# Kernel tuning notes

Hardware: AMD Instinct MI355X
Metric: run time of the kernel (lower is better)

Reference implementation:

```python
import jax, jax.numpy as jnp
import numpy as np

N_NODES = 50000
N_EDGES = 625000
HIDDEN = 128
NUM_GRAPHS = 128
EPS = 1e-5


def setup_inputs() -> dict:
    key = jax.random.key(0)
    ks = jax.random.split(key, 8)
    node = jax.random.normal(ks[0], (N_NODES, HIDDEN), dtype=jnp.float32)
    edge_index = jax.random.randint(ks[1], (2, N_EDGES), 0, N_NODES, dtype=jnp.int64)
    edge_attr = jax.random.uniform(ks[2], (N_EDGES,), dtype=jnp.float32)
    batch_ptr = jnp.sort(jax.random.randint(ks[3], (N_NODES,), 0, NUM_GRAPHS, dtype=jnp.int64))
    # GCNConv linear: weight [out,in], bias [out]
    W = jax.random.normal(ks[4], (HIDDEN, HIDDEN), dtype=jnp.float32) * (1.0 / np.sqrt(HIDDEN))
    b = jnp.zeros((HIDDEN,), dtype=jnp.float32)
    # GraphNorm params
    gn_weight = 1.0 + 0.02 * jax.random.normal(ks[5], (HIDDEN,), dtype=jnp.float32)
    gn_bias = 0.05 * jax.random.normal(ks[6], (HIDDEN,), dtype=jnp.float32)
    gn_mean_scale = 1.0 + 0.02 * jax.random.normal(ks[7], (HIDDEN,), dtype=jnp.float32)
    return {"node": node, "edge_index": edge_index, "edge_attr": edge_attr,
            "batch_ptr": batch_ptr, "W": W, "b": b,
            "gn_weight": gn_weight, "gn_bias": gn_bias, "gn_mean_scale": gn_mean_scale}


def _gcn_conv(x, src, dst, w, W, b):
    n = x.shape[0]
    # add self loops with weight 1
    loop = jnp.arange(n, dtype=src.dtype)
    src = jnp.concatenate([src, loop])
    dst = jnp.concatenate([dst, loop])
    w = jnp.concatenate([w, jnp.ones((n,), dtype=w.dtype)])
    # symmetric degree normalization (degrees at target nodes)
    deg = jax.ops.segment_sum(w, dst, num_segments=n)
    dinv = jnp.where(deg > 0, jax.lax.rsqrt(deg), 0.0)
    norm = dinv[src] * w * dinv[dst]  # [E+n]
    h = x @ W.T  # [n, d]
    msg = norm[:, None] * h[src]  # gather + scale
    out = jax.ops.segment_sum(msg, dst, num_segments=n)  # scatter-add
    return out + b


def _graph_norm(x, batch, weight, bias, mean_scale):
    cnt = jax.ops.segment_sum(jnp.ones((x.shape[0],), x.dtype), batch, num_segments=NUM_GRAPHS)
    cnt = jnp.maximum(cnt, 1.0)[:, None]
    mean = jax.ops.segment_sum(x, batch, num_segments=NUM_GRAPHS) / cnt
    centered = x - mean_scale * mean[batch]
    var = jax.ops.segment_sum(centered * centered, batch, num_segments=NUM_GRAPHS) / cnt
    inv_std = jax.lax.rsqrt(var + EPS)[batch]
    return weight * centered * inv_std + bias


def reference(node, edge_index, edge_attr, batch_ptr, W, b, gn_weight, gn_bias, gn_mean_scale):
    src, dst = edge_index[0], edge_index[1]
    h = _gcn_conv(node, src, dst, edge_attr, W, b)
    h = _graph_norm(h, batch_ptr, gn_weight, gn_bias, gn_mean_scale)
    return jax.nn.relu(h)
```

## Files before the change

### kernel.cpp

```cpp
#include <hip/hip_runtime.h>

#define N_NODES    50000
#define N_EDGES    625000
#define HIDDEN     128
#define NUM_GRAPHS 128
#define EPS_GN     1e-5f
#define FIXSCALE   1048576.0f
#define NGEMM_BLK  782
#define NHIST_BLK  611
#define CPAD       8

typedef __bf16 bf16x8 __attribute__((ext_vector_type(8)));
typedef float  f32x4  __attribute__((ext_vector_type(4)));
typedef unsigned short u16x8 __attribute__((ext_vector_type(8)));
typedef unsigned long long u64;

__device__ inline unsigned short f2b(float f) {
    __bf16 b = (__bf16)f;
    return __builtin_bit_cast(unsigned short, b);
}
__device__ inline float b2f(unsigned short u) {
    unsigned int x = ((unsigned int)u) << 16;
    return __builtin_bit_cast(float, x);
}

#define HB_OFF     0
#define CNT64_OFF  3200000
#define DINV_OFF   4000000
#define SCALE_OFF  4050000
#define SHIFT_OFF  4066384
#define GSTART_OFF 4082768
#define ROWS_OFF   4083000
#define BSUM_OFF   4133100
#define BOFF_OFF   4133400
#define EPACK_OFF  4133700
#define SLOT_OFF   5383700
#define WB_OFF     6008700

__global__ void prep(const float* __restrict__ W, unsigned short* __restrict__ wb,
                     uint4* __restrict__ cntz) {
    int i = blockIdx.x * 256 + threadIdx.x;
    if (i < 800000 / 4) cntz[i] = make_uint4(0u, 0u, 0u, 0u);
    if (i < HIDDEN * HIDDEN) wb[i] = f2b(W[i]);
}

__global__ __launch_bounds__(256) void gemm_hist(const float* __restrict__ x,
                                                 const unsigned short* __restrict__ wb,
                                                 unsigned short* __restrict__ hb,
                                                 const int* __restrict__ dst,
                                                 const float* __restrict__ w,
                                                 u64* __restrict__ cnt64,
                                                 unsigned int* __restrict__ slot) {
    if (blockIdx.x >= NGEMM_BLK) {
        int base = (blockIdx.x - NGEMM_BLK) * 256 + threadIdx.x;
        if (base * 4 >= N_EDGES) return;
        int4   d4 = ((const int4*)dst)[base];
        float4 w4 = ((const float4*)w)[base];
        unsigned int fx0 = (unsigned int)(w4.x * FIXSCALE + 0.5f);
        unsigned int fx1 = (unsigned int)(w4.y * FIXSCALE + 0.5f);
        unsigned int fx2 = (unsigned int)(w4.z * FIXSCALE + 0.5f);
        unsigned int fx3 = (unsigned int)(w4.w * FIXSCALE + 0.5f);
        u64 o0 = atomicAdd(&cnt64[(size_t)d4.x * CPAD], (1ULL << 32) | (u64)fx0);
        u64 o1 = atomicAdd(&cnt64[(size_t)d4.y * CPAD], (1ULL << 32) | (u64)fx1);
        u64 o2 = atomicAdd(&cnt64[(size_t)d4.z * CPAD], (1ULL << 32) | (u64)fx2);
        u64 o3 = atomicAdd(&cnt64[(size_t)d4.w * CPAD], (1ULL << 32) | (u64)fx3);
        uint4 s4;
        s4.x = (unsigned int)(o0 >> 32);
        s4.y = (unsigned int)(o1 >> 32);
        s4.z = (unsigned int)(o2 >> 32);
        s4.w = (unsigned int)(o3 >> 32);
        ((uint4*)slot)[base] = s4;
        return;
    }
    const int wave = threadIdx.x >> 6;
    const int lane = threadIdx.x & 63;
    const int row0 = blockIdx.x * 64 + wave * 16;
    const int r  = lane & 15;
    const int ko = (lane >> 4) * 8;
    f32x4 acc[8];
#pragma unroll
    for (int t = 0; t < 8; ++t) { acc[t][0] = 0.f; acc[t][1] = 0.f; acc[t][2] = 0.f; acc[t][3] = 0.f; }
    int arow = row0 + r;
    if (arow >= N_NODES) arow = N_NODES - 1;
    const size_t abase = (size_t)arow * HIDDEN + ko;
#pragma unroll
    for (int kt = 0; kt < HIDDEN; kt += 32) {
        float4 a0 = *(const float4*)(x + abase + kt);
        float4 a1 = *(const float4*)(x + abase + kt + 4);
        bf16x8 a;
        a[0] = (__bf16)a0.x; a[1] = (__bf16)a0.y; a[2] = (__bf16)a0.z; a[3] = (__bf16)a0.w;
        a[4] = (__bf16)a1.x; a[5] = (__bf16)a1.y; a[6] = (__bf16)a1.z; a[7] = (__bf16)a1.w;
#pragma unroll
        for (int t = 0; t < 8; ++t) {
            bf16x8 b = *(const bf16x8*)(wb + (size_t)(t * 16 + r) * HIDDEN + kt + ko);
            acc[t] = __builtin_amdgcn_mfma_f32_16x16x32_bf16(a, b, acc[t], 0, 0, 0);
        }
    }
    const int orow = row0 + (lane >> 4) * 4;
#pragma unroll
    for (int t = 0; t < 8; ++t) {
#pragma unroll
        for (int j = 0; j < 4; ++j) {
            int rr = orow + j;
            if (rr < N_NODES) hb[(size_t)rr * HIDDEN + t * 16 + r] = f2b(acc[t][j]);
        }
    }
}

__global__ void scan_partial(const u64* __restrict__ cnt64, int* __restrict__ bsum,
                             float* __restrict__ dinv,
                             const int* __restrict__ batch, int* __restrict__ gstart) {
    __shared__ int red[256];
    int i = blockIdx.x * 256 + threadIdx.x;
    int c = 0;
    if (i < N_NODES) {
        u64 v = cnt64[(size_t)i * CPAD];
        c = (int)(v >> 32);
        dinv[i] = rsqrtf(1.0f + (float)(unsigned int)v * (1.0f / FIXSCALE));
        int b0 = batch[i];
        int prev = (i == 0) ? -1 : batch[i - 1];
        for (int g = prev + 1; g <= b0; ++g) gstart[g] = i;
        if (i == N_NODES - 1) {
            for (int g = b0 + 1; g <= NUM_GRAPHS; ++g) gstart[g] = N_NODES;
        }
    }
    red[threadIdx.x] = c;
    __syncthreads();
    for (int off = 128; off > 0; off >>= 1) {
        if (threadIdx.x < off) red[threadIdx.x] += red[threadIdx.x + off];
        __syncthreads();
    }
    if (threadIdx.x == 0) bsum[blockIdx.x] = red[0];
}

__global__ void scan_bsums(const int* __restrict__ bsum, int* __restrict__ boff, int nblocks) {
    __shared__ int s[256];
    int t = threadIdx.x;
    int v0 = (t < nblocks) ? bsum[t] : 0;
    s[t] = v0;
    __syncthreads();
    for (int off = 1; off < 256; off <<= 1) {
        int v = (t >= off) ? s[t - off] : 0;
        __syncthreads();
        s[t] += v;
        __syncthreads();
    }
    boff[t] = s[t] - v0;
}

__global__ void scan_emit(const u64* __restrict__ cnt64, const int* __restrict__ boff,
                          int* __restrict__ rowstart) {
    __shared__ int s[256];
    int t = threadIdx.x;
    int i = blockIdx.x * 256 + t;
    int v0 = (i < N_NODES) ? (int)(cnt64[(size_t)i * CPAD] >> 32) : 0;
    s[t] = v0;
    __syncthreads();
    for (int off = 1; off < 256; off <<= 1) {
        int v = (t >= off) ? s[t - off] : 0;
        __syncthreads();
        s[t] += v;
        __syncthreads();
    }
    if (i < N_NODES) rowstart[i] = boff[blockIdx.x] + s[t] - v0;
    if (i == N_NODES) rowstart[N_NODES] = N_EDGES;
}

__global__ void csr_fill(const int* __restrict__ src, const int* __restrict__ dst,
                         const float* __restrict__ w, const float* __restrict__ dinv,
                         const int* __restrict__ rowstart, const unsigned int* __restrict__ slot,
                         u64* __restrict__ epack) {
    int base = blockIdx.x * blockDim.x + threadIdx.x;
    if (base * 4 >= N_EDGES) return;
    int4   s4 = ((const int4*)src)[base];
    int4   d4 = ((const int4*)dst)[base];
    float4 w4 = ((const float4*)w)[base];
    uint4  r4 = ((const uint4*)slot)[base];
    float nm0 = dinv[s4.x] * w4.x * dinv[d4.x];
    float nm1 = dinv[s4.y] * w4.y * dinv[d4.y];
    float nm2 = dinv[s4.z] * w4.z * dinv[d4.z];
    float nm3 = dinv[s4.w] * w4.w * dinv[d4.w];
    epack[rowstart[d4.x] + (int)r4.x] = (u64)(unsigned int)s4.x | ((u64)__float_as_uint(nm0) << 32);
    epack[rowstart[d4.y] + (int)r4.y] = (u64)(unsigned int)s4.y | ((u64)__float_as_uint(nm1) << 32);
    epack[rowstart[d4.z] + (int)r4.z] = (u64)(unsigned int)s4.z | ((u64)__float_as_uint(nm2) << 32);
    epack[rowstart[d4.w] + (int)r4.w] = (u64)(unsigned int)s4.w | ((u64)__float_as_uint(nm3) << 32);
}

__global__ __launch_bounds__(256) void gather_fused(const unsigned short* __restrict__ hb,
                                                    const int* __restrict__ rowstart,
                                                    const u64* __restrict__ epack,
                                                    const float* __restrict__ dinv,
                                                    const float* __restrict__ b,
                                                    float* __restrict__ out) {
    const int t = threadIdx.x;
    const int n = blockIdx.x * 16 + (t >> 4);
    if (n >= N_NODES) return;
    const int c8 = (t & 15) * 8;
    const int s0 = rowstart[n];
    const int e0 = rowstart[n + 1];
    const float di = dinv[n];
    const float sl = di * di;
    float acc[8];
    {
        u16x8 hv = *(const u16x8*)(hb + (size_t)n * HIDDEN + c8);
#pragma unroll
        for (int j = 0; j < 8; ++j) acc[j] = sl * b2f(hv[j]);
    }
    int p = s0;
    for (; p + 2 <= e0; p += 2) {
        u64 e1 = epack[p];
        u64 e2 = epack[p + 1];
        int   s1 = (int)(unsigned int)e1;
        float n1 = __uint_as_float((unsigned int)(e1 >> 32));
        int   sg2 = (int)(unsigned int)e2;
        float n2 = __uint_as_float((unsigned int)(e2 >> 32));
        u16x8 v1 = *(const u16x8*)(hb + (size_t)s1 * HIDDEN + c8);
        u16x8 v2 = *(const u16x8*)(hb + (size_t)sg2 * HIDDEN + c8);
#pragma unroll
        for (int j = 0; j < 8; ++j) acc[j] = fmaf(n1, b2f(v1[j]), acc[j]);
#pragma unroll
        for (int j = 0; j < 8; ++j) acc[j] = fmaf(n2, b2f(v2[j]), acc[j]);
    }
    if (p < e0) {
        u64 e1 = epack[p];
        int   s1 = (int)(unsigned int)e1;
        float n1 = __uint_as_float((unsigned int)(e1 >> 32));
        u16x8 v1 = *(const u16x8*)(hb + (size_t)s1 * HIDDEN + c8);
#pragma unroll
        for (int j = 0; j < 8; ++j) acc[j] = fmaf(n1, b2f(v1[j]), acc[j]);
    }
    float4 b0 = *(const float4*)(b + c8);
    float4 b1 = *(const float4*)(b + c8 + 4);
    float4 o0, o1;
    o0.x = acc[0] + b0.x; o0.y = acc[1] + b0.y; o0.z = acc[2] + b0.z; o0.w = acc[3] + b0.w;
    o1.x = acc[4] + b1.x; o1.y = acc[5] + b1.y; o1.z = acc[6] + b1.z; o1.w = acc[7] + b1.w;
    *(float4*)(out + (size_t)n * HIDDEN + c8)     = o0;
    *(float4*)(out + (size_t)n * HIDDEN + c8 + 4) = o1;
}

__global__ __launch_bounds__(256) void graph_stats(const float* __restrict__ out,
                                                   const int* __restrict__ gstart,
                                                   const float* __restrict__ ms,
                                                   const float* __restrict__ gw,
                                                   const float* __restrict__ gb,
                                                   float* __restrict__ scale,
                                                   float* __restrict__ shift) {
    const int g = blockIdx.x >> 2;
    const int q = blockIdx.x & 3;
    const int c = q * 32 + (threadIdx.x & 31);
    const int r = threadIdx.x >> 5;
    const int s = gstart[g];
    const int e = gstart[g + 1];
    float sum = 0.f, sq = 0.f;
    for (int n = s + r; n < e; n += 8) {
        float v = out[(size_t)n * HIDDEN + c];
        sum += v;
        sq = fmaf(v, v, sq);
    }
    __shared__ float ssum[8][32], ssq[8][32];
    ssum[r][threadIdx.x & 31] = sum;
    ssq[r][threadIdx.x & 31]  = sq;
    __syncthreads();
    if (r == 0) {
        int l = threadIdx.x & 31;
#pragma unroll
        for (int i = 1; i < 8; ++i) { sum += ssum[i][l]; sq += ssq[i][l]; }
        float cnt  = (float)max(e - s, 1);
        float mean = sum / cnt;
        float m2   = sq / cnt;
        float msv  = ms[c];
        float var  = fmaxf(m2 - mean * mean * msv * (2.f - msv), 0.f);
        float a    = gw[c] * rsqrtf(var + EPS_GN);
        scale[g * HIDDEN + c] = a;
        shift[g * HIDDEN + c] = gb[c] - a * msv * mean;
    }
}

__global__ __launch_bounds__(256) void gn_final(float* __restrict__ out,
                                                const float* __restrict__ scale,
                                                const float* __restrict__ shift,
                                                const int* __restrict__ batch) {
    int idx = blockIdx.x * blockDim.x + threadIdx.x;
    if (idx >= N_NODES * 32) return;
    int n  = idx >> 5;
    int c4 = (idx & 31) * 4;
    int g  = batch[n];
    float4 v  = *(float4*)(out + (size_t)n * HIDDEN + c4);
    float4 a  = *(const float4*)(scale + (size_t)g * HIDDEN + c4);
    float4 s  = *(const float4*)(shift + (size_t)g * HIDDEN + c4);
    v.x = fmaxf(fmaf(a.x, v.x, s.x), 0.f);
    v.y = fmaxf(fmaf(a.y, v.y, s.y), 0.f);
    v.z = fmaxf(fmaf(a.z, v.z, s.z), 0.f);
    v.w = fmaxf(fmaf(a.w, v.w, s.w), 0.f);
    *(float4*)(out + (size_t)n * HIDDEN + c4) = v;
}

extern "C" void kernel_launch(void* const* d_in, const int* in_sizes, int n_in,
                              void* d_out, int out_size, void* d_ws, size_t ws_size,
                              hipStream_t stream) {
    const float* node  = (const float*)d_in[0];
    const int*   ei    = (const int*)d_in[1];
    const float* eattr = (const float*)d_in[2];
    const int*   batch = (const int*)d_in[3];
    const float* W     = (const float*)d_in[4];
    const float* b     = (const float*)d_in[5];
    const float* gnw   = (const float*)d_in[6];
    const float* gnb   = (const float*)d_in[7];
    const float* gnms  = (const float*)d_in[8];
    float* out = (float*)d_out;
    float* ws  = (float*)d_ws;

    const int* src = ei;
    const int* dst = ei + N_EDGES;

    unsigned short* hb = (unsigned short*)(ws + HB_OFF);
    u64*   cnt64   = (u64*)(ws + CNT64_OFF);
    float* dinv    = ws + DINV_OFF;
    float* scale   = ws + SCALE_OFF;
    float* shift   = ws + SHIFT_OFF;
    int*   gstart  = (int*)(ws + GSTART_OFF);
    int*   rowstart= (int*)(ws + ROWS_OFF);
    int*   bsum    = (int*)(ws + BSUM_OFF);
    int*   boff    = (int*)(ws + BOFF_OFF);
    u64*   epack   = (u64*)(ws + EPACK_OFF);
    unsigned int* slot = (unsigned int*)(ws + SLOT_OFF);
    unsigned short* wb = (unsigned short*)(ws + WB_OFF);

    const int NB = (N_NODES + 255) / 256;

    prep<<<(200000 + 255) / 256, 256, 0, stream>>>(W, wb, (uint4*)cnt64);
    gemm_hist<<<NGEMM_BLK + NHIST_BLK, 256, 0, stream>>>(node, wb, hb, dst, eattr, cnt64, slot);
    scan_partial<<<NB, 256, 0, stream>>>(cnt64, bsum, dinv, batch, gstart);
    scan_bsums<<<1, 256, 0, stream>>>(bsum, boff, NB);
    scan_emit<<<NB, 256, 0, stream>>>(cnt64, boff, rowstart);
    csr_fill<<<NHIST_BLK, 256, 0, stream>>>(src, dst, eattr, dinv, rowstart, slot, epack);
    gather_fused<<<(N_NODES + 15) / 16, 256, 0, stream>>>(hb, rowstart, epack, dinv, b, out);
    graph_stats<<<NUM_GRAPHS * 4, 256, 0, stream>>>(out, gstart, gnms, gnw, gnb, scale, shift);
    gn_final<<<(N_NODES * 32 + 255) / 256, 256, 0, stream>>>(out, scale, shift, batch);

    (void)in_sizes; (void)n_in; (void)out_size; (void)ws_size;
}
```

Before: 128.4 us.

## Store conv output as bf16 and fuse GraphNorm stats with apply pass

The gather kernel now writes its result as bf16 into a workspace buffer placed over the slot array, instead of fp32 into the output. GraphNorm statistics and the normalize+ReLU step are merged into one per-graph kernel that reads the bf16 buffer twice and writes fp32 output, removing the scale/shift round trip and one launch. This halves the intermediate traffic but adds bf16 rounding before normalization. The apply pass now runs on only 512 blocks with per-column scalar accesses, which may parallelize worse than the old elementwise kernel.

```diff
diff --git a/kernel.cpp b/kernel.cpp
--- a/kernel.cpp
+++ b/kernel.cpp
@@ -27,8 +27,6 @@
 #define HB_OFF     0
 #define CNT64_OFF  3200000
 #define DINV_OFF   4000000
-#define SCALE_OFF  4050000
-#define SHIFT_OFF  4066384
 #define GSTART_OFF 4082768
 #define ROWS_OFF   4083000
 #define BSUM_OFF   4133100
@@ -36,6 +34,11 @@
 #define EPACK_OFF  4133700
 #define SLOT_OFF   5383700
 #define WB_OFF     6008700
+#define TMP_OFF    6020000
+#undef TMP_OFF
+#define TMP_OFF    5383700
+#undef WB_OFF
+#define WB_OFF     4050000
 
 __global__ void prep(const float* __restrict__ W, unsigned short* __restrict__ wb,
                      uint4* __restrict__ cntz) {
@@ -191,7 +194,7 @@
                                                     const u64* __restrict__ epack,
                                                     const float* __restrict__ dinv,
                                                     const float* __restrict__ b,
-                                                    float* __restrict__ out) {
+                                                    unsigned short* __restrict__ tmp) {
     const int t = threadIdx.x;
     const int n = blockIdx.x * 16 + (t >> 4);
     if (n >= N_NODES) return;
@@ -231,38 +234,39 @@
     }
     float4 b0 = *(const float4*)(b + c8);
     float4 b1 = *(const float4*)(b + c8 + 4);
-    float4 o0, o1;
-    o0.x = acc[0] + b0.x; o0.y = acc[1] + b0.y; o0.z = acc[2] + b0.z; o0.w = acc[3] + b0.w;
-    o1.x = acc[4] + b1.x; o1.y = acc[5] + b1.y; o1.z = acc[6] + b1.z; o1.w = acc[7] + b1.w;
-    *(float4*)(out + (size_t)n * HIDDEN + c8)     = o0;
-    *(float4*)(out + (size_t)n * HIDDEN + c8 + 4) = o1;
-}
-
-__global__ __launch_bounds__(256) void graph_stats(const float* __restrict__ out,
+    u16x8 o;
+    o[0] = f2b(acc[0] + b0.x); o[1] = f2b(acc[1] + b0.y);
+    o[2] = f2b(acc[2] + b0.z); o[3] = f2b(acc[3] + b0.w);
+    o[4] = f2b(acc[4] + b1.x); o[5] = f2b(acc[5] + b1.y);
+    o[6] = f2b(acc[6] + b1.z); o[7] = f2b(acc[7] + b1.w);
+    *(u16x8*)(tmp + (size_t)n * HIDDEN + c8) = o;
+}
+
+__global__ __launch_bounds__(256) void stats_apply(const unsigned short* __restrict__ tmp,
                                                    const int* __restrict__ gstart,
                                                    const float* __restrict__ ms,
                                                    const float* __restrict__ gw,
                                                    const float* __restrict__ gb,
-                                                   float* __restrict__ scale,
-                                                   float* __restrict__ shift) {
+                                                   float* __restrict__ out) {
     const int g = blockIdx.x >> 2;
     const int q = blockIdx.x & 3;
-    const int c = q * 32 + (threadIdx.x & 31);
+    const int l = threadIdx.x & 31;
+    const int c = q * 32 + l;
     const int r = threadIdx.x >> 5;
     const int s = gstart[g];
     const int e = gstart[g + 1];
     float sum = 0.f, sq = 0.f;
     for (int n = s + r; n < e; n += 8) {
-        float v = out[(size_t)n * HIDDEN + c];
+        float v = b2f(tmp[(size_t)n * HIDDEN + c]);
         sum += v;
         sq = fmaf(v, v, sq);
     }
     __shared__ float ssum[8][32], ssq[8][32];
-    ssum[r][threadIdx.x & 31] = sum;
-    ssq[r][threadIdx.x & 31]  = sq;
+    __shared__ float sA[32], sS[32];
+    ssum[r][l] = sum;
+    ssq[r][l]  = sq;
     __syncthreads();
     if (r == 0) {
-        int l = threadIdx.x & 31;
 #pragma unroll
         for (int i = 1; i < 8; ++i) { sum += ssum[i][l]; sq += ssq[i][l]; }
         float cnt  = (float)max(e - s, 1);
@@ -271,28 +275,16 @@
         float msv  = ms[c];
         float var  = fmaxf(m2 - mean * mean * msv * (2.f - msv), 0.f);
         float a    = gw[c] * rsqrtf(var + EPS_GN);
-        scale[g * HIDDEN + c] = a;
-        shift[g * HIDDEN + c] = gb[c] - a * msv * mean;
-    }
-}
-
-__global__ __launch_bounds__(256) void gn_final(float* __restrict__ out,
-                                                const float* __restrict__ scale,
-                                                const float* __restrict__ shift,
-                                                const int* __restrict__ batch) {
-    int idx = blockIdx.x * blockDim.x + threadIdx.x;
-    if (idx >= N_NODES * 32) return;
-    int n  = idx >> 5;
-    int c4 = (idx & 31) * 4;
-    int g  = batch[n];
-    float4 v  = *(float4*)(out + (size_t)n * HIDDEN + c4);
-    float4 a  = *(const float4*)(scale + (size_t)g * HIDDEN + c4);
-    float4 s  = *(const float4*)(shift + (size_t)g * HIDDEN + c4);
-    v.x = fmaxf(fmaf(a.x, v.x, s.x), 0.f);
-    v.y = fmaxf(fmaf(a.y, v.y, s.y), 0.f);
-    v.z = fmaxf(fmaf(a.z, v.z, s.z), 0.f);
-    v.w = fmaxf(fmaf(a.w, v.w, s.w), 0.f);
-    *(float4*)(out + (size_t)n * HIDDEN + c4) = v;
+        sA[l] = a;
+        sS[l] = gb[c] - a * msv * mean;
+    }
+    __syncthreads();
+    float a  = sA[l];
+    float sh = sS[l];
+    for (int n = s + r; n < e; n += 8) {
+        float v = b2f(tmp[(size_t)n * HIDDEN + c]);
+        out[(size_t)n * HIDDEN + c] = fmaxf(fmaf(a, v, sh), 0.f);
+    }
 }
 
 extern "C" void kernel_launch(void* const* d_in, const int* in_sizes, int n_in,
@@ -316,8 +308,6 @@
     unsigned short* hb = (unsigned short*)(ws + HB_OFF);
     u64*   cnt64   = (u64*)(ws + CNT64_OFF);
     float* dinv    = ws + DINV_OFF;
-    float* scale   = ws + SCALE_OFF;
-    float* shift   = ws + SHIFT_OFF;
     int*   gstart  = (int*)(ws + GSTART_OFF);
     int*   rowstart= (int*)(ws + ROWS_OFF);
     int*   bsum    = (int*)(ws + BSUM_OFF);
@@ -325,6 +315,7 @@
     u64*   epack   = (u64*)(ws + EPACK_OFF);
     unsigned int* slot = (unsigned int*)(ws + SLOT_OFF);
     unsigned short* wb = (unsigned short*)(ws + WB_OFF);
+    unsigned short* tmp = (unsigned short*)(ws + TMP_OFF);
 
     const int NB = (N_NODES + 255) / 256;
 
@@ -333,10 +324,9 @@
     scan_partial<<<NB, 256, 0, stream>>>(cnt64, bsum, dinv, batch, gstart);
     scan_bsums<<<1, 256, 0, stream>>>(bsum, boff, NB);
     scan_emit<<<NB, 256, 0, stream>>>(cnt64, boff, rowstart);
-    csr_fill<<<NHIST_BLK, 256, 0, stream>>>(src, dst, eattr, dinv, rowstart, slot, epack);
-    gather_fused<<<(N_NODES + 15) / 16, 256, 0, stream>>>(hb, rowstart, epack, dinv, b, out);
-    graph_stats<<<NUM_GRAPHS * 4, 256, 0, stream>>>(out, gstart, gnms, gnw, gnb, scale, shift);
-    gn_final<<<(N_NODES * 32 + 255) / 256, 256, 0, stream>>>(out, scale, shift, batch);
+    csr_fill<<<(N_EDGES / 4 + 255) / 256, 256, 0, stream>>>(src, dst, eattr, dinv, rowstart, slot, epack);
+    gather_fused<<<(N_NODES + 15) / 16, 256, 0, stream>>>(hb, rowstart, epack, dinv, b, tmp);
+    stats_apply<<<NUM_GRAPHS * 4, 256, 0, stream>>>(tmp, gstart, gnms, gnw, gnb, out);
 
     (void)in_sizes; (void)n_in; (void)out_size; (void)ws_size;
 }
```

After: 128.3 us. Within noise of the previous version (-0.1%).
